# Optimization experiments

Measured on AMD Instinct MI355X. Metric: run time of the kernel, lower is better.

The kernel has to match this reference:

```python
import jax, jax.numpy as jnp
import numpy as np

T, N, IN, H, OUT, B = 250, 256, 1024, 1024, 35, 4
IN_B = IN // B
V_TH = 1.0  # spikingjelly LIFNode defaults: v_threshold=1.0, v_reset=0.0, decay_input=True


def heaviside(x):
    return (x >= 0.0).astype(x.dtype)


def setup_inputs() -> dict:
    key = jax.random.key(0)
    ks = jax.random.split(key, 9)
    x = jax.random.normal(ks[0], (T, N, IN), dtype=jnp.float32)
    # branch Linear(IN_B, H) stacked over branches: weight [B, IN_B, H], bias [B, H]
    Wb = jax.random.normal(ks[1], (B, IN_B, H), dtype=jnp.float32) / np.sqrt(IN_B)
    bb = jax.random.normal(ks[2], (B, H), dtype=jnp.float32) * 0.01
    # branch_taus ~ U(2, 6), shape [B, H]
    taus = jax.random.uniform(ks[3], (B, H), dtype=jnp.float32, minval=2.0, maxval=6.0)
    W2 = jax.random.normal(ks[4], (H, OUT), dtype=jnp.float32) / np.sqrt(H)
    b2 = jax.random.normal(ks[5], (OUT,), dtype=jnp.float32) * 0.01
    # learnable membrane time constants ~ U(0.5, 4) (clipped away from 0 for stability)
    tau1 = jax.random.uniform(ks[6], (1,), dtype=jnp.float32, minval=0.5, maxval=4.0)
    tau2 = jax.random.uniform(ks[7], (1,), dtype=jnp.float32, minval=0.5, maxval=4.0)
    return {"x": x, "Wb": Wb, "bb": bb, "taus": taus, "W2": W2, "b2": b2,
            "tau1": tau1, "tau2": tau2}


def reference(x, Wb, bb, taus, W2, b2, tau1, tau2):
    alpha = jax.nn.sigmoid(taus)  # [B, H] dendritic leak gates

    def step(carry, x_t):
        state, v1, v2, acc = carry
        # split input into contiguous branch chunks: [N, B, IN_B]
        xr = x_t.reshape(N, B, IN_B)
        branch_in = jnp.einsum('nbi,bih->nbh', xr, Wb) + bb  # [N, B, H]
        state = alpha * state + (1.0 - alpha) * branch_in     # leaky dendritic integration
        combined = state.sum(axis=1)                          # [N, H]
        # LIF1: charge (decay_input), fire (heaviside), hard reset (detach_reset)
        v1 = v1 + (combined - v1) / tau1
        s1 = heaviside(v1 - V_TH)
        v1 = v1 * (1.0 - s1)
        h2 = s1 @ W2 + b2                                     # [N, OUT]
        v2 = v2 + (h2 - v2) / tau2
        s2 = heaviside(v2 - V_TH)
        v2 = v2 * (1.0 - s2)
        return (state, v1, v2, acc + s2), None

    init = (jnp.zeros((N, B, H), x.dtype), jnp.zeros((N, H), x.dtype),
            jnp.zeros((N, OUT), x.dtype), jnp.zeros((N, OUT), x.dtype))
    (_, _, _, out_sum), _ = jax.lax.scan(step, init, x)
    return jax.nn.log_softmax(out_sum, axis=1)
```

## Files before the change

### kernel.cpp

```cpp
#include <hip/hip_runtime.h>
#include <cstdint>
#include <cstddef>


typedef __bf16 bf16;
typedef __bf16 bf16x8 __attribute__((ext_vector_type(8)));
typedef float  f32x4  __attribute__((ext_vector_type(4)));

#define Tt    250
#define Nn    256
#define Hh    1024
#define OUTK  35
#define NBR   4

#define OFF_FLAG 0u
#define OFF_WBT  256u
#define OFF_W2T  2097408u
#define OFF_ALF  2195712u
#define OFF_OMF  2212096u
#define OFF_BBF  2228480u
#define OFF_B2S  2244864u
#define OFF_H2   2245120u
#define OFF_STW  14533120u
#define OFF_V1W  18727424u
#define OFF_S1P  19776000u
#define OFF_BIN  27968000u
#define FIXED_WS 27968000u

__device__ __forceinline__ float ld_in(const void* p, size_t i, int f32) {
    return f32 ? ((const float*)p)[i] : (float)((const bf16*)p)[i];
}

__device__ __forceinline__ void gload16(const void* g, void* l) {
    __builtin_amdgcn_global_load_lds(
        (const __attribute__((address_space(1))) void*)g,
        (__attribute__((address_space(3))) void*)l, 16, 0, 0);
}

__global__ void sniff_kernel(const unsigned short* __restrict__ x,
                             int* __restrict__ flag) {
    int cnt = 0;
    for (int i = threadIdx.x; i < 4096; i += 64) {
        int e = (x[i] >> 7) & 0xFF;
        cnt += (e >= 100 && e <= 140) ? 1 : 0;
    }
#pragma unroll
    for (int o = 32; o > 0; o >>= 1) cnt += __shfl_xor(cnt, o);
    if (threadIdx.x == 0) *flag = (cnt < 3400) ? 1 : 0;
}

__global__ void trans_wb_kernel(const void* __restrict__ Wb, bf16* __restrict__ WbT,
                                const int* __restrict__ flagp) {
    int f32 = *flagp;
    __shared__ bf16 tile[32][33];
    int bid = blockIdx.x;
    int b   = bid >> 8;
    int rem = bid & 255;
    int kt  = rem >> 5;
    int htl = rem & 31;
    int tx = threadIdx.x & 31, ty = threadIdx.x >> 5;
#pragma unroll
    for (int i = 0; i < 4; ++i) {
        int k = kt * 32 + ty + i * 8;
        int h = htl * 32 + tx;
        tile[ty + i * 8][tx] = (bf16)ld_in(Wb, (size_t)(b * 256 + k) * 1024 + h, f32);
    }
    __syncthreads();
#pragma unroll
    for (int i = 0; i < 4; ++i) {
        int h = htl * 32 + ty + i * 8;
        int k = kt * 32 + tx;
        WbT[((size_t)b * 1024 + h) * 256 + k] = tile[tx][ty + i * 8];
    }
}

__global__ void trans_w2_kernel(const void* __restrict__ W2, bf16* __restrict__ W2T,
                                const int* __restrict__ flagp) {
    int f32 = *flagp;
    int idx = blockIdx.x * 256 + threadIdx.x;
    int c = idx >> 10;
    int k = idx & 1023;
    W2T[idx] = (c < OUTK) ? (bf16)ld_in(W2, (size_t)k * OUTK + c, f32) : (bf16)0.0f;
}

__global__ void prep_kernel(const void* taus, const void* bb, const void* b2,
                            const void* tau1, const void* tau2,
                            float* alf, float* omf, float* bbf, float* b2s,
                            const int* __restrict__ flagp) {
    int f32 = *flagp;
    int idx = blockIdx.x * 256 + threadIdx.x;
    if (idx < 4096) {
        float tv = ld_in(taus, idx, f32);
        float a = 1.0f / (1.0f + expf(-tv));
        alf[idx] = a;
        omf[idx] = 1.0f - a;
        bbf[idx] = ld_in(bb, idx, f32);
    } else if (idx < 4144) {
        int c = idx - 4096;
        b2s[c] = (c < OUTK) ? ld_in(b2, c, f32) : 0.0f;
    } else if (idx == 4144) {
        b2s[48] = ld_in(tau1, 0, f32);
    } else if (idx == 4145) {
        b2s[49] = ld_in(tau2, 0, f32);
    }
}

__global__ __launch_bounds__(256, 2)
void gemm1_kernel(const void* __restrict__ xsrc,
                  const bf16* __restrict__ BT, bf16* __restrict__ C,
                  const int* __restrict__ flagp, int TCl) {
    __shared__ bf16 Alds[4096];
    __shared__ bf16 Blds[4096];
    int f32 = *flagp;
    int tid = threadIdx.x;
    int tiles_pb = TCl * 16;
    int branch = blockIdx.x / tiles_pb;
    int rem = blockIdx.x % tiles_pb;
    int mt = rem >> 3, ht = rem & 7;
    int w = tid >> 6, lane = tid & 63;
    int l15 = lane & 15, l4 = lane >> 4;
    int wm = w >> 1, wh = w & 1;
    const int m0 = mt * 128, h0 = ht * 128;

    f32x4 zero = {0.f, 0.f, 0.f, 0.f};
    f32x4 acc[4][4];
#pragma unroll
    for (int mi = 0; mi < 4; ++mi)
#pragma unroll
        for (int hi = 0; hi < 4; ++hi) acc[mi][hi] = zero;

    const bf16* Bbase = BT + (size_t)branch * (1024 * 256) + (size_t)h0 * 256;
    const int row = tid >> 2;
    const int ce = (tid & 3) * 8;

    for (int kc = 0; kc < 8; ++kc) {
        bf16x8 av[2];
#pragma unroll
        for (int r = 0; r < 2; ++r) {
            size_t gi = (size_t)(m0 + r * 64 + row) * 1024 + branch * 256 + kc * 32 + ce;
            if (f32) {
                const float4* p = (const float4*)((const float*)xsrc + gi);
                float4 u0 = p[0], u1 = p[1];
                av[r][0] = (bf16)u0.x; av[r][1] = (bf16)u0.y;
                av[r][2] = (bf16)u0.z; av[r][3] = (bf16)u0.w;
                av[r][4] = (bf16)u1.x; av[r][5] = (bf16)u1.y;
                av[r][6] = (bf16)u1.z; av[r][7] = (bf16)u1.w;
            } else {
                av[r] = *(const bf16x8*)((const bf16*)xsrc + gi);
            }
        }
        __syncthreads();
#pragma unroll
        for (int r = 0; r < 2; ++r) {
            gload16(Bbase + (size_t)(r * 64 + row) * 256 + kc * 32 + ce,
                    &Blds[(size_t)(r * 256 + tid) * 8]);
            *(bf16x8*)&Alds[(size_t)(r * 256 + tid) * 8] = av[r];
        }
        __syncthreads();
        bf16x8 af[4], bfr[4];
#pragma unroll
        for (int mi = 0; mi < 4; ++mi)
            af[mi] = *(const bf16x8*)&Alds[(wm * 64 + mi * 16 + l15) * 32 + l4 * 8];
#pragma unroll
        for (int hi = 0; hi < 4; ++hi)
            bfr[hi] = *(const bf16x8*)&Blds[(wh * 64 + hi * 16 + l15) * 32 + l4 * 8];
#pragma unroll
        for (int mi = 0; mi < 4; ++mi)
#pragma unroll
            for (int hi = 0; hi < 4; ++hi)
                acc[mi][hi] = __builtin_amdgcn_mfma_f32_16x16x32_bf16(
                    af[mi], bfr[hi], acc[mi][hi], 0, 0, 0);
        __syncthreads();
    }

    bf16* Cb = C + (size_t)branch * ((size_t)TCl * 256 * 1024);
#pragma unroll
    for (int mi = 0; mi < 4; ++mi)
#pragma unroll
        for (int hi = 0; hi < 4; ++hi) {
            int rr = m0 + wm * 64 + mi * 16 + l4 * 4;
            int col = h0 + wh * 64 + hi * 16 + l15;
#pragma unroll
            for (int r = 0; r < 4; ++r)
                Cb[(size_t)(rr + r) * 1024 + col] = (bf16)acc[mi][hi][r];
        }
}

template<int TCC>
__global__ void scan_kernel(const bf16* __restrict__ bin,
                            const float* __restrict__ alf,
                            const float* __restrict__ omf,
                            const float* __restrict__ bbf,
                            const float* __restrict__ b2s,
                            unsigned long long* __restrict__ s1p,
                            float* __restrict__ stw,
                            float* __restrict__ v1w,
                            int t0, int TCl_rt) {
    const int TCl = TCC ? TCC : TCl_rt;
    int n = blockIdx.x >> 2;
    int h = (blockIdx.x & 3) * 256 + threadIdx.x;
    int lane = threadIdx.x & 63;
    int widx = (blockIdx.x & 3) * 4 + (threadIdx.x >> 6);
    size_t CHEc = (size_t)TCl * 256 * 1024;
    size_t base = (size_t)n * 1024 + h;

    float al[NBR], om[NBR], bbv[NBR], st[NBR];
    float v1;
#pragma unroll
    for (int b = 0; b < NBR; ++b) {
        al[b] = alf[b * Hh + h];
        om[b] = omf[b * Hh + h];
        bbv[b] = bbf[b * Hh + h];
    }
    if (t0 == 0) {
#pragma unroll
        for (int b = 0; b < NBR; ++b) st[b] = 0.f;
        v1 = 0.f;
    } else {
#pragma unroll
        for (int b = 0; b < NBR; ++b)
            st[b] = stw[((size_t)b * Nn + n) * Hh + h];
        v1 = v1w[(size_t)n * Hh + h];
    }
    float tau1 = b2s[48];

    float nxt[NBR];
#pragma unroll
    for (int b = 0; b < NBR; ++b) nxt[b] = (float)bin[b * CHEc + base];

#pragma unroll 2
    for (int tl = 0; tl < TCl; ++tl) {
        float cur[NBR];
#pragma unroll
        for (int b = 0; b < NBR; ++b) cur[b] = nxt[b];
        if (tl + 1 < TCl) {
            size_t nb = base + (size_t)(tl + 1) * (256 * 1024);
#pragma unroll
            for (int b = 0; b < NBR; ++b) nxt[b] = (float)bin[b * CHEc + nb];
        }
#pragma unroll
        for (int b = 0; b < NBR; ++b)
            st[b] = al[b] * st[b] + om[b] * (cur[b] + bbv[b]);
        float comb = st[0] + st[1] + st[2] + st[3];
        v1 += (comb - v1) / tau1;
        bool sp = (v1 >= 1.0f);
        unsigned long long m = __ballot(sp);
        if (lane == 0)
            s1p[((size_t)(t0 + tl) * Nn + n) * 16 + widx] = m;
        if (sp) v1 = 0.f;
    }
#pragma unroll
    for (int b = 0; b < NBR; ++b) stw[((size_t)b * Nn + n) * Hh + h] = st[b];
    v1w[(size_t)n * Hh + h] = v1;
}

__global__ __launch_bounds__(256, 2)
void gemm2_kernel(const unsigned char* __restrict__ s1b,
                  const bf16* __restrict__ W2T, float* __restrict__ h2) {
    __shared__ bf16 Alds[4096];
    __shared__ bf16 Blds[1536];
    int tid = threadIdx.x;
    int m0 = blockIdx.x * 128;
    int w = tid >> 6, lane = tid & 63;
    int l15 = lane & 15, l4 = lane >> 4;

    f32x4 zero = {0.f, 0.f, 0.f, 0.f};
    f32x4 acc[2][3];
#pragma unroll
    for (int mi = 0; mi < 2; ++mi)
#pragma unroll
        for (int hi = 0; hi < 3; ++hi) acc[mi][hi] = zero;

    const bf16 ONE = (bf16)1.0f, ZER = (bf16)0.0f;

    for (int kc = 0; kc < 32; ++kc) {
        bf16x8 av[2], bv;
#pragma unroll
        for (int r = 0; r < 2; ++r) {
            int L = r * 256 + tid;
            int row = L >> 2;
            unsigned char bits = s1b[(size_t)(m0 + row) * 128 + kc * 4 + (L & 3)];
#pragma unroll
            for (int j = 0; j < 8; ++j)
                av[r][j] = ((bits >> j) & 1) ? ONE : ZER;
        }
        if (tid < 192)
            bv = *(const bf16x8*)&W2T[(size_t)(tid >> 2) * 1024 + kc * 32 + (tid & 3) * 8];
        __syncthreads();
#pragma unroll
        for (int r = 0; r < 2; ++r)
            *(bf16x8*)&Alds[(size_t)(r * 256 + tid) * 8] = av[r];
        if (tid < 192)
            *(bf16x8*)&Blds[(size_t)tid * 8] = bv;
        __syncthreads();
        bf16x8 af[2], bfr[3];
#pragma unroll
        for (int mi = 0; mi < 2; ++mi)
            af[mi] = *(const bf16x8*)&Alds[(w * 32 + mi * 16 + l15) * 32 + l4 * 8];
#pragma unroll
        for (int hi = 0; hi < 3; ++hi)
            bfr[hi] = *(const bf16x8*)&Blds[(hi * 16 + l15) * 32 + l4 * 8];
#pragma unroll
        for (int mi = 0; mi < 2; ++mi)
#pragma unroll
            for (int hi = 0; hi < 3; ++hi)
                acc[mi][hi] = __builtin_amdgcn_mfma_f32_16x16x32_bf16(
                    af[mi], bfr[hi], acc[mi][hi], 0, 0, 0);
        __syncthreads();
    }
#pragma unroll
    for (int mi = 0; mi < 2; ++mi)
#pragma unroll
        for (int hi = 0; hi < 3; ++hi) {
            int col = hi * 16 + l15;
#pragma unroll
            for (int r = 0; r < 4; ++r) {
                int m = m0 + w * 32 + mi * 16 + l4 * 4 + r;
                int t = m >> 8;
                int n = m & 255;
                h2[((size_t)n * Tt + t) * 48 + col] = acc[mi][hi][r];
            }
        }
}

__global__ void out_kernel(const float* __restrict__ h2,
                           const float* __restrict__ b2s,
                           float* __restrict__ out) {
    int n = blockIdx.x;
    int k = threadIdx.x;
    float b2v = (k < 48) ? b2s[k] : 0.f;
    float tau2 = b2s[49];
    float v2 = 0.f, acc = 0.f;
    const float* base = h2 + (size_t)n * Tt * 48;
    for (int t = 0; t < Tt; ++t) {
        float hv = (k < 48) ? base[t * 48 + k] : 0.f;
        hv += b2v;
        v2 += (hv - v2) / tau2;
        bool sp = (v2 >= 1.0f);
        if (sp) { acc += 1.f; v2 = 0.f; }
    }
    float val = (k < OUTK) ? acc : -3.0e38f;
    float mx = val;
#pragma unroll
    for (int o = 32; o > 0; o >>= 1) mx = fmaxf(mx, __shfl_xor(mx, o));
    float e = (k < OUTK) ? expf(val - mx) : 0.f;
    float s = e;
#pragma unroll
    for (int o = 32; o > 0; o >>= 1) s += __shfl_xor(s, o);
    if (k < OUTK) out[n * OUTK + k] = (val - mx) - logf(s);
}

extern "C" void kernel_launch(void* const* d_in, const int* in_sizes, int n_in,
                              void* d_out, int out_size, void* d_ws, size_t ws_size,
                              hipStream_t stream) {
    const void* x    = d_in[0];
    const void* Wb   = d_in[1];
    const void* bb   = d_in[2];
    const void* taus = d_in[3];
    const void* W2   = d_in[4];
    const void* b2   = d_in[5];
    const void* tau1 = d_in[6];
    const void* tau2 = d_in[7];
    float* out = (float*)d_out;

    char* ws = (char*)d_ws;
    int*   flag = (int*)(ws + OFF_FLAG);
    bf16*  WbT  = (bf16*)(ws + OFF_WBT);
    bf16*  W2T  = (bf16*)(ws + OFF_W2T);
    float* alf  = (float*)(ws + OFF_ALF);
    float* omf  = (float*)(ws + OFF_OMF);
    float* bbf  = (float*)(ws + OFF_BBF);
    float* b2s  = (float*)(ws + OFF_B2S);
    float* h2   = (float*)(ws + OFF_H2);
    float* stw  = (float*)(ws + OFF_STW);
    float* v1w  = (float*)(ws + OFF_V1W);
    unsigned long long* s1p = (unsigned long long*)(ws + OFF_S1P);
    bf16*  bin  = (bf16*)(ws + OFF_BIN);

    const int cands[8] = {250, 125, 50, 25, 10, 5, 2, 1};
    int TC = 1;
    for (int i = 0; i < 8; ++i) {
        size_t need = (size_t)FIXED_WS + (size_t)cands[i] * 2097152u;
        if (need <= ws_size) { TC = cands[i]; break; }
    }

    sniff_kernel<<<1, 64, 0, stream>>>((const unsigned short*)x, flag);
    trans_wb_kernel<<<1024, 256, 0, stream>>>(Wb, WbT, flag);
    trans_w2_kernel<<<192, 256, 0, stream>>>(W2, W2T, flag);
    prep_kernel<<<17, 256, 0, stream>>>(taus, bb, b2, tau1, tau2,
                                        alf, omf, bbf, b2s, flag);

    int nch = Tt / TC;
    for (int c = 0; c < nch; ++c) {
        const void* xc = (const void*)((const char*)x +
            (size_t)c * TC * 256 * 1024 * 4);
        gemm1_kernel<<<64 * TC, 256, 0, stream>>>(xc, WbT, bin, flag, TC);
        if (TC == 250)
            scan_kernel<250><<<1024, 256, 0, stream>>>(
                bin, alf, omf, bbf, b2s, s1p, stw, v1w, c * TC, TC);
        else
            scan_kernel<0><<<1024, 256, 0, stream>>>(
                bin, alf, omf, bbf, b2s, s1p, stw, v1w, c * TC, TC);
    }
    gemm2_kernel<<<500, 256, 0, stream>>>((const unsigned char*)s1p, W2T, h2);
    out_kernel<<<Nn, 64, 0, stream>>>(h2, b2s, out);

    (void)in_sizes; (void)n_in; (void)out_size;
}
```

Measured before the change: 1.022 ms.

## Double-buffer gemm1 LDS tiles with XOR swizzle and grouped tile remap

The branch-GEMM kernel now keeps two LDS buffers and prefetches the next K-chunk of A and B from global memory while MFMAs run on the current one, with one barrier per iteration instead of three. LDS writes and reads use an XOR swizzle on the 8-element column group to cut bank conflicts. Block indices are also remapped in groups of eight to change L2 locality. The cost is double the LDS footprint and more live registers for the prefetched fp32 data, which may hurt occupancy at two blocks per CU.

```diff
diff --git a/kernel.cpp b/kernel.cpp
--- a/kernel.cpp
+++ b/kernel.cpp
@@ -109,19 +109,29 @@
 void gemm1_kernel(const void* __restrict__ xsrc,
                   const bf16* __restrict__ BT, bf16* __restrict__ C,
                   const int* __restrict__ flagp, int TCl) {
-    __shared__ bf16 Alds[4096];
-    __shared__ bf16 Blds[4096];
+    __shared__ bf16 Alds[2][4096];
+    __shared__ bf16 Blds[2][4096];
     int f32 = *flagp;
     int tid = threadIdx.x;
     int tiles_pb = TCl * 16;
-    int branch = blockIdx.x / tiles_pb;
-    int rem = blockIdx.x % tiles_pb;
+
+    int nwg = gridDim.x;
+    int bid = blockIdx.x;
+    int tile = ((nwg & 7) == 0) ? ((bid & 7) * (nwg >> 3) + (bid >> 3)) : bid;
+
+    int branch = tile / tiles_pb;
+    int rem = tile % tiles_pb;
     int mt = rem >> 3, ht = rem & 7;
     int w = tid >> 6, lane = tid & 63;
     int l15 = lane & 15, l4 = lane >> 4;
     int wm = w >> 1, wh = w & 1;
     const int m0 = mt * 128, h0 = ht * 128;
 
+    const int row = tid >> 2;
+    const int q   = tid & 3;
+    const int swr = (tid >> 3) & 3;
+    const int srd = (l15 >> 1) & 3;
+
     f32x4 zero = {0.f, 0.f, 0.f, 0.f};
     f32x4 acc[4][4];
 #pragma unroll
@@ -130,47 +140,85 @@
         for (int hi = 0; hi < 4; ++hi) acc[mi][hi] = zero;
 
     const bf16* Bbase = BT + (size_t)branch * (1024 * 256) + (size_t)h0 * 256;
-    const int row = tid >> 2;
-    const int ce = (tid & 3) * 8;
-
+
+    float4 anxt[2][2];
+    bf16x8 bnxt[2];
+
+    auto issueB = [&](int kc, int pp) {
+#pragma unroll
+        for (int r = 0; r < 2; ++r)
+            gload16(Bbase + (size_t)(r * 64 + row) * 256 + kc * 32 + (q ^ swr) * 8,
+                    &Blds[pp][(size_t)(r * 256 + tid) * 8]);
+    };
+    auto issueA = [&](int kc) {
+        if (f32) {
+#pragma unroll
+            for (int r = 0; r < 2; ++r) {
+                const float4* pa = (const float4*)((const float*)xsrc +
+                    ((size_t)(m0 + r * 64 + row) * 1024 + branch * 256 + kc * 32 + q * 8));
+                anxt[r][0] = pa[0];
+                anxt[r][1] = pa[1];
+            }
+        } else {
+#pragma unroll
+            for (int r = 0; r < 2; ++r)
+                bnxt[r] = *(const bf16x8*)((const bf16*)xsrc +
+                    ((size_t)(m0 + r * 64 + row) * 1024 + branch * 256 + kc * 32 + q * 8));
+        }
+    };
+    auto writeA = [&](int pp) {
+#pragma unroll
+        for (int r = 0; r < 2; ++r) {
+            bf16x8 av;
+            if (f32) {
+                float4 u0 = anxt[r][0], u1 = anxt[r][1];
+                av[0] = (bf16)u0.x; av[1] = (bf16)u0.y;
+                av[2] = (bf16)u0.z; av[3] = (bf16)u0.w;
+                av[4] = (bf16)u1.x; av[5] = (bf16)u1.y;
+                av[6] = (bf16)u1.z; av[7] = (bf16)u1.w;
+            } else {
+                av = bnxt[r];
+            }
+            *(bf16x8*)&Alds[pp][(size_t)(r * 64 + row) * 32 + (q ^ swr) * 8] = av;
+        }
+    };
+
+    issueB(0, 0);
+    issueA(0);
+    asm volatile("s_waitcnt vmcnt(0)" ::: "memory");
+    writeA(0);
+    asm volatile("s_waitcnt lgkmcnt(0)" ::: "memory");
+    __builtin_amdgcn_s_barrier();
+
+#pragma unroll
     for (int kc = 0; kc < 8; ++kc) {
-        bf16x8 av[2];
-#pragma unroll
-        for (int r = 0; r < 2; ++r) {
-            size_t gi = (size_t)(m0 + r * 64 + row) * 1024 + branch * 256 + kc * 32 + ce;
-            if (f32) {
-                const float4* p = (const float4*)((const float*)xsrc + gi);
-                float4 u0 = p[0], u1 = p[1];
-                av[r][0] = (bf16)u0.x; av[r][1] = (bf16)u0.y;
-                av[r][2] = (bf16)u0.z; av[r][3] = (bf16)u0.w;
-                av[r][4] = (bf16)u1.x; av[r][5] = (bf16)u1.y;
-                av[r][6] = (bf16)u1.z; av[r][7] = (bf16)u1.w;
-            } else {
-                av[r] = *(const bf16x8*)((const bf16*)xsrc + gi);
-            }
-        }
-        __syncthreads();
-#pragma unroll
-        for (int r = 0; r < 2; ++r) {
-            gload16(Bbase + (size_t)(r * 64 + row) * 256 + kc * 32 + ce,
-                    &Blds[(size_t)(r * 256 + tid) * 8]);
-            *(bf16x8*)&Alds[(size_t)(r * 256 + tid) * 8] = av[r];
-        }
-        __syncthreads();
+        const int p = kc & 1;
+        if (kc < 7) {
+            issueB(kc + 1, p ^ 1);
+            issueA(kc + 1);
+        }
+        __builtin_amdgcn_sched_barrier(0);
         bf16x8 af[4], bfr[4];
 #pragma unroll
         for (int mi = 0; mi < 4; ++mi)
-            af[mi] = *(const bf16x8*)&Alds[(wm * 64 + mi * 16 + l15) * 32 + l4 * 8];
+            af[mi] = *(const bf16x8*)&Alds[p][(wm * 64 + mi * 16 + l15) * 32 + (l4 ^ srd) * 8];
 #pragma unroll
         for (int hi = 0; hi < 4; ++hi)
-            bfr[hi] = *(const bf16x8*)&Blds[(wh * 64 + hi * 16 + l15) * 32 + l4 * 8];
+            bfr[hi] = *(const bf16x8*)&Blds[p][(wh * 64 + hi * 16 + l15) * 32 + (l4 ^ srd) * 8];
 #pragma unroll
         for (int mi = 0; mi < 4; ++mi)
 #pragma unroll
             for (int hi = 0; hi < 4; ++hi)
                 acc[mi][hi] = __builtin_amdgcn_mfma_f32_16x16x32_bf16(
                     af[mi], bfr[hi], acc[mi][hi], 0, 0, 0);
-        __syncthreads();
+        if (kc < 7) {
+            asm volatile("s_waitcnt vmcnt(0)" ::: "memory");
+            writeA(p ^ 1);
+            asm volatile("s_waitcnt lgkmcnt(0)" ::: "memory");
+        } else {
+            asm volatile("s_waitcnt lgkmcnt(0)" ::: "memory");
+        }
+        __builtin_amdgcn_s_barrier();
     }
 
     bf16* Cb = C + (size_t)branch * ((size_t)TCl * 256 * 1024);
```

After: 899.1 us. 12.0% less time.

## Load GEMM1 fragments directly to registers with double buffering and prefetch scan inputs

Applied to the files above, without the earlier changes.

GEMM1 no longer stages A and B tiles through LDS. Each wave loads its MFMA fragments straight from global memory into double-buffered registers, which removes the per-k barriers, and block IDs are remapped for L2 locality. The scan kernel now prefetches two timesteps ahead and out_kernel prefetches the next h2 value. In exchange, operands are no longer shared across waves, so each tile is loaded redundantly from global memory and register pressure rises.

```diff
diff --git a/kernel.cpp b/kernel.cpp
--- a/kernel.cpp
+++ b/kernel.cpp
@@ -31,10 +31,11 @@
     return f32 ? ((const float*)p)[i] : (float)((const bf16*)p)[i];
 }
 
-__device__ __forceinline__ void gload16(const void* g, void* l) {
-    __builtin_amdgcn_global_load_lds(
-        (const __attribute__((address_space(1))) void*)g,
-        (__attribute__((address_space(3))) void*)l, 16, 0, 0);
+__device__ __forceinline__ bf16x8 cvt8(float4 u0, float4 u1) {
+    bf16x8 r;
+    r[0] = (bf16)u0.x; r[1] = (bf16)u0.y; r[2] = (bf16)u0.z; r[3] = (bf16)u0.w;
+    r[4] = (bf16)u1.x; r[5] = (bf16)u1.y; r[6] = (bf16)u1.z; r[7] = (bf16)u1.w;
+    return r;
 }
 
 __global__ void sniff_kernel(const unsigned short* __restrict__ x,
@@ -109,13 +110,16 @@
 void gemm1_kernel(const void* __restrict__ xsrc,
                   const bf16* __restrict__ BT, bf16* __restrict__ C,
                   const int* __restrict__ flagp, int TCl) {
-    __shared__ bf16 Alds[4096];
-    __shared__ bf16 Blds[4096];
     int f32 = *flagp;
     int tid = threadIdx.x;
     int tiles_pb = TCl * 16;
-    int branch = blockIdx.x / tiles_pb;
-    int rem = blockIdx.x % tiles_pb;
+
+    int nwg = gridDim.x;
+    int bid = blockIdx.x;
+    int tile = ((nwg & 7) == 0) ? ((bid & 7) * (nwg >> 3) + (bid >> 3)) : bid;
+
+    int branch = tile / tiles_pb;
+    int rem = tile % tiles_pb;
     int mt = rem >> 3, ht = rem & 7;
     int w = tid >> 6, lane = tid & 63;
     int l15 = lane & 15, l4 = lane >> 4;
@@ -129,48 +133,46 @@
 #pragma unroll
         for (int hi = 0; hi < 4; ++hi) acc[mi][hi] = zero;
 
-    const bf16* Bbase = BT + (size_t)branch * (1024 * 256) + (size_t)h0 * 256;
-    const int row = tid >> 2;
-    const int ce = (tid & 3) * 8;
-
+    const size_t aoff = (size_t)(m0 + wm * 64 + l15) * 1024 + branch * 256 + l4 * 8;
+    const float* xA32 = (const float*)xsrc + aoff;
+    const bf16*  xA16 = (const bf16*)xsrc + aoff;
+    const bf16*  Bp   = BT + (size_t)branch * (1024 * 256)
+                          + (size_t)(h0 + wh * 64 + l15) * 256 + l4 * 8;
+
+    bf16x8 A[2][4], Bf[2][4];
+
+    auto loadA = [&](int buf, int kc) {
+#pragma unroll
+        for (int mi = 0; mi < 4; ++mi) {
+            if (f32) {
+                const float4* p = (const float4*)(xA32 + (size_t)mi * 16 * 1024 + kc * 32);
+                A[buf][mi] = cvt8(p[0], p[1]);
+            } else {
+                A[buf][mi] = *(const bf16x8*)(xA16 + (size_t)mi * 16 * 1024 + kc * 32);
+            }
+        }
+    };
+    auto loadB = [&](int buf, int kc) {
+#pragma unroll
+        for (int hi = 0; hi < 4; ++hi)
+            Bf[buf][hi] = *(const bf16x8*)(Bp + (size_t)hi * 16 * 256 + kc * 32);
+    };
+
+    loadA(0, 0);
+    loadB(0, 0);
+#pragma unroll
     for (int kc = 0; kc < 8; ++kc) {
-        bf16x8 av[2];
-#pragma unroll
-        for (int r = 0; r < 2; ++r) {
-            size_t gi = (size_t)(m0 + r * 64 + row) * 1024 + branch * 256 + kc * 32 + ce;
-            if (f32) {
-                const float4* p = (const float4*)((const float*)xsrc + gi);
-                float4 u0 = p[0], u1 = p[1];
-                av[r][0] = (bf16)u0.x; av[r][1] = (bf16)u0.y;
-                av[r][2] = (bf16)u0.z; av[r][3] = (bf16)u0.w;
-                av[r][4] = (bf16)u1.x; av[r][5] = (bf16)u1.y;
-                av[r][6] = (bf16)u1.z; av[r][7] = (bf16)u1.w;
-            } else {
-                av[r] = *(const bf16x8*)((const bf16*)xsrc + gi);
-            }
-        }
-        __syncthreads();
-#pragma unroll
-        for (int r = 0; r < 2; ++r) {
-            gload16(Bbase + (size_t)(r * 64 + row) * 256 + kc * 32 + ce,
-                    &Blds[(size_t)(r * 256 + tid) * 8]);
-            *(bf16x8*)&Alds[(size_t)(r * 256 + tid) * 8] = av[r];
-        }
-        __syncthreads();
-        bf16x8 af[4], bfr[4];
-#pragma unroll
-        for (int mi = 0; mi < 4; ++mi)
-            af[mi] = *(const bf16x8*)&Alds[(wm * 64 + mi * 16 + l15) * 32 + l4 * 8];
-#pragma unroll
-        for (int hi = 0; hi < 4; ++hi)
-            bfr[hi] = *(const bf16x8*)&Blds[(wh * 64 + hi * 16 + l15) * 32 + l4 * 8];
+        const int cur = kc & 1, nxt = cur ^ 1;
+        if (kc < 7) {
+            loadA(nxt, kc + 1);
+            loadB(nxt, kc + 1);
+        }
 #pragma unroll
         for (int mi = 0; mi < 4; ++mi)
 #pragma unroll
             for (int hi = 0; hi < 4; ++hi)
                 acc[mi][hi] = __builtin_amdgcn_mfma_f32_16x16x32_bf16(
-                    af[mi], bfr[hi], acc[mi][hi], 0, 0, 0);
-        __syncthreads();
+                    A[cur][mi], Bf[cur][hi], acc[mi][hi], 0, 0, 0);
     }
 
     bf16* Cb = C + (size_t)branch * ((size_t)TCl * 256 * 1024);
@@ -224,19 +226,24 @@
     }
     float tau1 = b2s[48];
 
-    float nxt[NBR];
-#pragma unroll
-    for (int b = 0; b < NBR; ++b) nxt[b] = (float)bin[b * CHEc + base];
+    float nxt[2][NBR];
+#pragma unroll
+    for (int b = 0; b < NBR; ++b) nxt[0][b] = (float)bin[b * CHEc + base];
+    if (TCl > 1) {
+#pragma unroll
+        for (int b = 0; b < NBR; ++b)
+            nxt[1][b] = (float)bin[b * CHEc + base + (size_t)(256 * 1024)];
+    }
 
 #pragma unroll 2
     for (int tl = 0; tl < TCl; ++tl) {
         float cur[NBR];
 #pragma unroll
-        for (int b = 0; b < NBR; ++b) cur[b] = nxt[b];
-        if (tl + 1 < TCl) {
-            size_t nb = base + (size_t)(tl + 1) * (256 * 1024);
-#pragma unroll
-            for (int b = 0; b < NBR; ++b) nxt[b] = (float)bin[b * CHEc + nb];
+        for (int b = 0; b < NBR; ++b) cur[b] = nxt[tl & 1][b];
+        if (tl + 2 < TCl) {
+            size_t nb = base + (size_t)(tl + 2) * (256 * 1024);
+#pragma unroll
+            for (int b = 0; b < NBR; ++b) nxt[tl & 1][b] = (float)bin[b * CHEc + nb];
         }
 #pragma unroll
         for (int b = 0; b < NBR; ++b)
@@ -332,8 +339,10 @@
     float tau2 = b2s[49];
     float v2 = 0.f, acc = 0.f;
     const float* base = h2 + (size_t)n * Tt * 48;
+    float nx = (k < 48) ? base[k] : 0.f;
     for (int t = 0; t < Tt; ++t) {
-        float hv = (k < 48) ? base[t * 48 + k] : 0.f;
+        float hv = nx;
+        if (t + 1 < Tt) nx = (k < 48) ? base[(t + 1) * 48 + k] : 0.f;
         hv += b2v;
         v2 += (hv - v2) / tau2;
         bool sp = (v2 >= 1.0f);
```

Measured after the change: 1.305 ms. 1.28x slower.
